# Kernel optimization log

Measured on AMD Instinct MI355X. Metric: run time of the kernel, lower is better.

## Reference

```python
import jax, jax.numpy as jnp
import numpy as np
from jax import lax

B, S, D, T = 128, 512, 512, 64
OUT = 3


def setup_inputs() -> dict:
    key = jax.random.key(0)
    ks = jax.random.split(key, 16)
    sd = 0.05
    return {
        "e_all": jax.random.normal(ks[0], (B, S, D), jnp.float32),
        "e_last": jax.random.normal(ks[1], (1, B, D), jnp.float32),
        "target": jax.random.normal(ks[2], (B, T, OUT), jnp.float32),
        # attention params
        "Wa": jax.random.normal(ks[3], (D, D), jnp.float32) * sd,
        "ba": jnp.zeros((D,), jnp.float32),
        "Ua": jax.random.normal(ks[4], (D, D), jnp.float32) * sd,
        "bu": jnp.zeros((D,), jnp.float32),
        "Va_w": jax.random.normal(ks[5], (1, D), jnp.float32) * sd,
        "Va_b": jnp.zeros((1,), jnp.float32),
        # GRU params (PyTorch layout: [3D, in], gates order r,z,n)
        "W_ih": jax.random.normal(ks[6], (3 * D, D + OUT), jnp.float32) * sd,
        "b_ih": jnp.zeros((3 * D,), jnp.float32),
        "W_hh": jax.random.normal(ks[7], (3 * D, D), jnp.float32) * sd,
        "b_hh": jnp.zeros((3 * D,), jnp.float32),
        # output projection
        "W_out": jax.random.normal(ks[8], (OUT, D), jnp.float32) * sd,
        "b_out": jnp.zeros((OUT,), jnp.float32),
    }


def reference(e_all, e_last, target, Wa, ba, Ua, bu, Va_w, Va_b,
              W_ih, b_ih, W_hh, b_hh, W_out, b_out):
    # Precompute Ua(keys): keys are fixed across timesteps (same math as per-step).
    Uk = jnp.einsum('bsd,ed->bse', e_all, Ua) + bu        # [B,S,D]
    va = Va_w[0]                                          # [D]

    def step(h, x):
        # h: [B,D] decoder hidden; x: [B,3] decoder input (dropout is eval/identity)
        q = h @ Wa.T + ba                                  # [B,D]
        scores = jnp.einsum('bsd,d->bs', jnp.tanh(q[:, None, :] + Uk), va) + Va_b[0]
        w = jax.nn.softmax(scores, axis=-1)                # [B,S]
        ctx = jnp.einsum('bs,bsd->bd', w, e_all)           # [B,D]
        gin = jnp.concatenate([ctx, x], axis=-1)           # [B,D+3]  (attn first)
        gi = gin @ W_ih.T + b_ih                           # [B,3D]
        gh = h @ W_hh.T + b_hh                             # [B,3D]
        i_r, i_z, i_n = jnp.split(gi, 3, axis=-1)
        h_r, h_z, h_n = jnp.split(gh, 3, axis=-1)
        r = jax.nn.sigmoid(i_r + h_r)
        z = jax.nn.sigmoid(i_z + h_z)
        n = jnp.tanh(i_n + r * h_n)
        h_new = (1.0 - z) * n + z * h                      # [B,D]
        out = h_new @ W_out.T + b_out                      # [B,3]
        return h_new, (out, w)

    # teacher forcing: step 0 sees zeros, step i sees target[:, i-1]
    xs = jnp.concatenate([jnp.zeros((1, B, OUT), e_all.dtype),
                          jnp.swapaxes(target[:, :T - 1, :], 0, 1)], axis=0)  # [T,B,3]
    hT, (outs, attns) = lax.scan(step, e_last[0], xs)
    d_outputs = jnp.swapaxes(outs, 0, 1)     # [B,T,3]
    cross_attn = jnp.swapaxes(attns, 0, 1)   # [B,T,S]
    return d_outputs, hT[None], cross_attn
```

## Files before the change

### kernel.cpp

```cpp
#include <hip/hip_runtime.h>
#include <cstdint>

constexpr int BB = 128;
constexpr int SS = 512;
constexpr int DD = 512;
constexpr int TT = 64;
constexpr int OO = 3;

typedef __attribute__((ext_vector_type(8))) short bf16x8;
typedef __attribute__((ext_vector_type(4))) float f32x4;

__device__ __forceinline__ float tanh_fast(float x) {
  float e = __expf(2.0f * x);
  return 1.0f - 2.0f / (e + 1.0f);
}
__device__ __forceinline__ float sigmoid_fast(float x) {
  return 1.0f / (1.0f + __expf(-x));
}
__device__ __forceinline__ unsigned short f2bf(float f) {
  uint32_t u = __float_as_uint(f);
  uint32_t r = (u + 0x7FFFu + ((u >> 16) & 1u)) >> 16;
  return (unsigned short)r;
}
__device__ __forceinline__ float2 bfx2(uint32_t u) {
  float2 r;
  r.x = __uint_as_float(u << 16);
  r.y = __uint_as_float(u & 0xFFFF0000u);
  return r;
}

template<int BM, int BN, int BK, int TM, int TN>
__device__ __forceinline__ void gemm_body(
    const float* __restrict__ A, int lda,
    const float* __restrict__ Bw, int ldb,
    const float* __restrict__ bias,
    float* __restrict__ C, int ldc, int K) {
  constexpr int TX = BN / TN, TY = BM / TM;
  static_assert(TX * TY == 256, "tile/thread mismatch");
  __shared__ float As[BK][BM + 4];
  __shared__ float Bs[BK][BN + 4];
  const int tid = threadIdx.x;
  const int bm = blockIdx.y * BM, bn = blockIdx.x * BN;
  const int tx = tid % TX, ty = tid / TX;
  float acc[TM][TN];
#pragma unroll
  for (int i = 0; i < TM; ++i)
#pragma unroll
    for (int j = 0; j < TN; ++j) acc[i][j] = 0.f;

  for (int k0 = 0; k0 < K; k0 += BK) {
#pragma unroll
    for (int i = 0; i < BM * BK / 256; ++i) {
      int idx = tid + i * 256;
      int m = idx / BK, k = idx % BK;
      As[k][m] = A[(size_t)(bm + m) * lda + k0 + k];
    }
#pragma unroll
    for (int i = 0; i < BN * BK / 256; ++i) {
      int idx = tid + i * 256;
      int n = idx / BK, k = idx % BK;
      Bs[k][n] = Bw[(size_t)(bn + n) * ldb + k0 + k];
    }
    __syncthreads();
#pragma unroll
    for (int k = 0; k < BK; ++k) {
      float ra[TM], rb[TN];
#pragma unroll
      for (int i = 0; i < TM; ++i) ra[i] = As[k][ty * TM + i];
#pragma unroll
      for (int j = 0; j < TN; ++j) rb[j] = Bs[k][tx * TN + j];
#pragma unroll
      for (int i = 0; i < TM; ++i)
#pragma unroll
        for (int j = 0; j < TN; ++j) acc[i][j] += ra[i] * rb[j];
    }
    __syncthreads();
  }
#pragma unroll
  for (int i = 0; i < TM; ++i) {
    int m = bm + ty * TM + i;
#pragma unroll
    for (int j = 0; j < TN; ++j) {
      int n = bn + tx * TN + j;
      C[(size_t)m * ldc + n] = acc[i][j] + bias[n];
    }
  }
}

__global__ __launch_bounds__(256) void gemm_uk_mfma(
    const unsigned short* __restrict__ A, const unsigned short* __restrict__ Bw,
    const float* __restrict__ bias, unsigned short* __restrict__ Uk) {
  __shared__ unsigned short Asb[128 * 40];
  __shared__ unsigned short Bsb[128 * 40];
  const int tid = threadIdx.x;
  const int m0 = blockIdx.y * 128, n0 = blockIdx.x * 128;
  const int w = tid >> 6, l = tid & 63;
  const int wr = w >> 1, wc = w & 1;
  const int lm = l & 15, kg = l >> 4;

  f32x4 acc[4][4] = {};

  for (int kc = 0; kc < 512; kc += 32) {
    uint4 av[2], bv[2];
#pragma unroll
    for (int p = 0; p < 2; ++p) {
      int u = tid + p * 256;
      int r = u >> 2, ko = (u & 3) * 8;
      av[p] = *(const uint4*)(A + (size_t)(m0 + r) * 512 + kc + ko);
      bv[p] = *(const uint4*)(Bw + (size_t)(n0 + r) * 512 + kc + ko);
    }
    __syncthreads();
#pragma unroll
    for (int p = 0; p < 2; ++p) {
      int u = tid + p * 256;
      int r = u >> 2, ko = (u & 3) * 8;
      *(uint4*)&Asb[r * 40 + ko] = av[p];
      *(uint4*)&Bsb[r * 40 + ko] = bv[p];
    }
    __syncthreads();
    bf16x8 af[4], bfr[4];
#pragma unroll
    for (int i = 0; i < 4; ++i) {
      af[i]  = *(const bf16x8*)&Asb[(wr * 64 + i * 16 + lm) * 40 + kg * 8];
      bfr[i] = *(const bf16x8*)&Bsb[(wc * 64 + i * 16 + lm) * 40 + kg * 8];
    }
#pragma unroll
    for (int i = 0; i < 4; ++i)
#pragma unroll
      for (int j = 0; j < 4; ++j)
        acc[i][j] = __builtin_amdgcn_mfma_f32_16x16x32_bf16(af[i], bfr[j],
                                                            acc[i][j], 0, 0, 0);
  }

  const int row_base = m0 + wr * 64;
  const int col_base = n0 + wc * 64;
#pragma unroll
  for (int j = 0; j < 4; ++j) {
    const int col = col_base + j * 16 + lm;
    const float bu = bias[col];
#pragma unroll
    for (int i = 0; i < 4; ++i) {
      const int r0 = row_base + i * 16 + kg * 4;
#pragma unroll
      for (int rr = 0; rr < 4; ++rr)
        Uk[(size_t)(r0 + rr) * 512 + col] = f2bf(acc[i][j][rr] + bu);
    }
  }
}

__global__ __launch_bounds__(256) void conv_bf(const float* __restrict__ in,
                                               unsigned short* __restrict__ outp) {
  size_t idx = ((size_t)blockIdx.x * 256 + threadIdx.x) * 8;
  const float4* p = (const float4*)(in + idx);
  float4 a = p[0], b = p[1];
  uint4 r;
  r.x = f2bf(a.x) | ((uint32_t)f2bf(a.y) << 16);
  r.y = f2bf(a.z) | ((uint32_t)f2bf(a.w) << 16);
  r.z = f2bf(b.x) | ((uint32_t)f2bf(b.y) << 16);
  r.w = f2bf(b.z) | ((uint32_t)f2bf(b.w) << 16);
  *(uint4*)(outp + idx) = r;
}

__global__ void prep_wcat(const float* __restrict__ Wa,
                          const float* __restrict__ Whh,
                          uint32_t* __restrict__ Wcat) {
  int idx = blockIdx.x * 256 + threadIdx.x;
  int k = idx >> 10, j2 = idx & 1023;
  int j0 = 2 * j2;
  float v0 = (j0 < DD) ? Wa[(size_t)j0 * DD + k] : Whh[(size_t)(j0 - DD) * DD + k];
  float v1 = (j0 + 1 < DD) ? Wa[(size_t)(j0 + 1) * DD + k]
                           : Whh[(size_t)(j0 + 1 - DD) * DD + k];
  Wcat[idx] = (uint32_t)f2bf(v0) | ((uint32_t)f2bf(v1) << 16);
}

__global__ void prep_bcat(const float* __restrict__ ba,
                          const float* __restrict__ bhh,
                          float* __restrict__ bcat) {
  int j = blockIdx.x * 256 + threadIdx.x;
  bcat[j] = (j < DD) ? ba[j] : bhh[j - DD];
}

__device__ __forceinline__ void qgh_gemm(
    const float* __restrict__ hn_sh, const uint32_t* __restrict__ Wcat,
    const float* __restrict__ bcat, float* __restrict__ q,
    float* __restrict__ gh, int b, int tid) {
  float2 acc = {0.f, 0.f};
#pragma unroll 8
  for (int k = 0; k < DD; ++k) {
    float2 wv = bfx2(Wcat[(size_t)k * 1024 + tid]);
    float hv = hn_sh[k];
    acc.x += hv * wv.x;
    acc.y += hv * wv.y;
  }
  const int j0 = 2 * tid;
  acc.x += bcat[j0];
  acc.y += bcat[j0 + 1];
  if (j0 < DD) {
    q[(size_t)b * DD + j0] = acc.x;
    q[(size_t)b * DD + j0 + 1] = acc.y;
  } else {
    gh[(size_t)b * 3 * DD + j0 - DD] = acc.x;
    gh[(size_t)b * 3 * DD + j0 + 1 - DD] = acc.y;
  }
}

__global__ __launch_bounds__(1024) void qgh_init(
    const float* __restrict__ e_last, const uint32_t* __restrict__ Wcat,
    const float* __restrict__ bcat, float* __restrict__ h,
    float* __restrict__ q, float* __restrict__ gh) {
  const int b = blockIdx.x, tid = threadIdx.x;
  __shared__ float hn[DD];
  if (tid < DD) {
    float v = e_last[(size_t)b * DD + tid];
    hn[tid] = v;
    h[(size_t)b * DD + tid] = v;
  }
  __syncthreads();
  qgh_gemm(hn, Wcat, bcat, q, gh, b, tid);
}

__global__ __launch_bounds__(256) void attn_scores(
    const unsigned short* __restrict__ Uk_bf, const float* __restrict__ q,
    const float* __restrict__ va, const float* __restrict__ vb_p,
    float* __restrict__ scores) {
  const int b = blockIdx.y;
  const int s0 = blockIdx.x * 64;
  __shared__ float4 shq[DD / 4];
  __shared__ float4 shva[DD / 4];
  const int tid = threadIdx.x;
  if (tid < DD / 4) {
    shq[tid] = ((const float4*)(q + (size_t)b * DD))[tid];
    shva[tid] = ((const float4*)va)[tid];
  }
  __syncthreads();
  const float vb = vb_p[0];
  const int g = tid >> 4, l = tid & 15;
#pragma unroll
  for (int i = 0; i < 4; ++i) {
    const int s = s0 + 16 * i + g;
    const uint4* row = (const uint4*)(Uk_bf + ((size_t)b * SS + s) * DD);
    float acc = 0.f;
#pragma unroll
    for (int jj = 0; jj < 4; ++jj) {
      const int slot = l + 16 * jj;
      uint4 u = row[slot];
      float4 q0 = shq[slot * 2], q1 = shq[slot * 2 + 1];
      float4 v0 = shva[slot * 2], v1 = shva[slot * 2 + 1];
      float2 e0 = bfx2(u.x), e1 = bfx2(u.y), e2 = bfx2(u.z), e3 = bfx2(u.w);
      acc += v0.x * tanh_fast(q0.x + e0.x);
      acc += v0.y * tanh_fast(q0.y + e0.y);
      acc += v0.z * tanh_fast(q0.z + e1.x);
      acc += v0.w * tanh_fast(q0.w + e1.y);
      acc += v1.x * tanh_fast(q1.x + e2.x);
      acc += v1.y * tanh_fast(q1.y + e2.y);
      acc += v1.z * tanh_fast(q1.z + e3.x);
      acc += v1.w * tanh_fast(q1.w + e3.y);
    }
#pragma unroll
    for (int off = 8; off; off >>= 1) acc += __shfl_down(acc, off, 16);
    if (l == 0) scores[(size_t)b * SS + s] = acc + vb;
  }
}

__global__ __launch_bounds__(256) void attn_ctx(
    const unsigned short* __restrict__ e_bf, const float* __restrict__ scores,
    float* __restrict__ ctx, float* __restrict__ attn_out, int t) {
  const int b = blockIdx.y, dc = blockIdx.x;
  __shared__ float w[SS];
  __shared__ float red[8];
  __shared__ float part[16][132];
  const int tid = threadIdx.x;

  float v0 = scores[(size_t)b * SS + tid];
  float v1 = scores[(size_t)b * SS + 256 + tid];
  float m = fmaxf(v0, v1);
#pragma unroll
  for (int off = 32; off; off >>= 1) m = fmaxf(m, __shfl_xor(m, off));
  if ((tid & 63) == 0) red[tid >> 6] = m;
  __syncthreads();
  m = fmaxf(fmaxf(red[0], red[1]), fmaxf(red[2], red[3]));
  float e0 = __expf(v0 - m), e1 = __expf(v1 - m);
  float ss = e0 + e1;
#pragma unroll
  for (int off = 32; off; off >>= 1) ss += __shfl_xor(ss, off);
  __syncthreads();
  if ((tid & 63) == 0) red[tid >> 6] = ss;
  __syncthreads();
  const float inv = 1.f / (red[0] + red[1] + red[2] + red[3]);
  float w0 = e0 * inv, w1 = e1 * inv;
  w[tid] = w0;
  w[tid + 256] = w1;
  if (dc == 0) {
    float* ao = attn_out + ((size_t)b * TT + t) * SS;
    ao[tid] = w0;
    ao[tid + 256] = w1;
  }
  __syncthreads();

  {
    const int sl = tid & 15, sg = tid >> 4;
    const unsigned short* eb = e_bf + (size_t)b * SS * DD + dc * 128 + sl * 8;
    float a0 = 0.f, a1 = 0.f, a2 = 0.f, a3 = 0.f;
    float a4 = 0.f, a5 = 0.f, a6 = 0.f, a7 = 0.f;
    for (int s = sg * 32; s < sg * 32 + 32; ++s) {
      uint4 u = *(const uint4*)(eb + (size_t)s * DD);
      float ws = w[s];
      float2 p0 = bfx2(u.x), p1 = bfx2(u.y), p2 = bfx2(u.z), p3 = bfx2(u.w);
      a0 += ws * p0.x; a1 += ws * p0.y;
      a2 += ws * p1.x; a3 += ws * p1.y;
      a4 += ws * p2.x; a5 += ws * p2.y;
      a6 += ws * p3.x; a7 += ws * p3.y;
    }
    float* pr = &part[sg][sl * 8];
    pr[0] = a0; pr[1] = a1; pr[2] = a2; pr[3] = a3;
    pr[4] = a4; pr[5] = a5; pr[6] = a6; pr[7] = a7;
  }
  __syncthreads();
  if (tid < 128) {
    const int sl = tid >> 3, c = tid & 7;
    float r = 0.f;
#pragma unroll
    for (int sg = 0; sg < 16; ++sg) r += part[sg][sl * 8 + c];
    ctx[(size_t)b * DD + dc * 128 + sl * 8 + c] = r;
  }
}

__global__ __launch_bounds__(256) void gi_gemm(
    const float* __restrict__ ctx, const float* __restrict__ W_ih,
    const float* __restrict__ bih, float* __restrict__ gi) {
  gemm_body<16, 64, 32, 1, 4>(ctx, DD, W_ih, DD + OO, bih, gi, 3 * DD, DD);
}

__global__ __launch_bounds__(1024) void update_fused(
    const float* __restrict__ gi, float* __restrict__ gh,
    float* __restrict__ h,
    const float* __restrict__ W_ih, const float* __restrict__ target,
    const float* __restrict__ W_out, const float* __restrict__ b_out,
    const uint32_t* __restrict__ Wcat, const float* __restrict__ bcat,
    float* __restrict__ q,
    float* __restrict__ out_d, float* __restrict__ out_hT, int t) {
  const int b = blockIdx.x, tid = threadIdx.x;
  __shared__ float hn[DD];
  const int wid = tid >> 6, lane = tid & 63;

  if (tid < DD) {
    const int d = tid;
    float x0 = 0.f, x1 = 0.f, x2 = 0.f;
    if (t > 0) {
      const float* xp = target + ((size_t)b * TT + (t - 1)) * OO;
      x0 = xp[0]; x1 = xp[1]; x2 = xp[2];
    }
    const float* gib = gi + (size_t)b * 3 * DD;
    const float* ghb = gh + (size_t)b * 3 * DD;
    const float* w0 = W_ih + (size_t)d * (DD + OO) + DD;
    const float* w1 = W_ih + (size_t)(DD + d) * (DD + OO) + DD;
    const float* w2 = W_ih + (size_t)(2 * DD + d) * (DD + OO) + DD;
    float ir  = gib[d]          + x0 * w0[0] + x1 * w0[1] + x2 * w0[2];
    float iz  = gib[DD + d]     + x0 * w1[0] + x1 * w1[1] + x2 * w1[2];
    float in_ = gib[2 * DD + d] + x0 * w2[0] + x1 * w2[1] + x2 * w2[2];
    float r = sigmoid_fast(ir + ghb[d]);
    float z = sigmoid_fast(iz + ghb[DD + d]);
    float n = tanh_fast(in_ + r * ghb[2 * DD + d]);
    float hp = h[(size_t)b * DD + d];
    float hnew = (1.f - z) * n + z * hp;
    h[(size_t)b * DD + d] = hnew;
    hn[d] = hnew;
    if (t == TT - 1) out_hT[(size_t)b * DD + d] = hnew;
  }
  __syncthreads();

  if (wid < OO) {
    const float* wrow = W_out + (size_t)wid * DD;
    float acc = 0.f;
    for (int i = lane; i < DD; i += 64) acc += hn[i] * wrow[i];
#pragma unroll
    for (int off = 32; off; off >>= 1) acc += __shfl_xor(acc, off);
    if (lane == 0) out_d[((size_t)b * TT + t) * OO + wid] = acc + b_out[wid];
  }

  qgh_gemm(hn, Wcat, bcat, q, gh, b, tid);
}

extern "C" void kernel_launch(void* const* d_in, const int* in_sizes, int n_in,
                              void* d_out, int out_size, void* d_ws, size_t ws_size,
                              hipStream_t stream) {
  const float* e_all  = (const float*)d_in[0];
  const float* e_last = (const float*)d_in[1];
  const float* target = (const float*)d_in[2];
  const float* Wa     = (const float*)d_in[3];
  const float* ba     = (const float*)d_in[4];
  const float* Ua     = (const float*)d_in[5];
  const float* bu     = (const float*)d_in[6];
  const float* Va_w   = (const float*)d_in[7];
  const float* Va_b   = (const float*)d_in[8];
  const float* W_ih   = (const float*)d_in[9];
  const float* b_ih   = (const float*)d_in[10];
  const float* W_hh   = (const float*)d_in[11];
  const float* b_hh   = (const float*)d_in[12];
  const float* W_out  = (const float*)d_in[13];
  const float* b_out  = (const float*)d_in[14];

  float* out      = (float*)d_out;
  float* out_d    = out;
  float* out_hT   = out + (size_t)BB * TT * OO;
  float* out_attn = out_hT + (size_t)BB * DD;

  char* wsB = (char*)d_ws;
  unsigned short* Uk_bf = (unsigned short*)wsB;
  unsigned short* e_bf  = (unsigned short*)(wsB + (size_t)BB * SS * DD * 2);
  uint32_t* Wcat = (uint32_t*)(wsB + (size_t)BB * SS * DD * 4);
  unsigned short* Ua_bf = (unsigned short*)(wsB + (size_t)BB * SS * DD * 4 +
                                            (size_t)DD * 2048 * 2);
  float* fws = (float*)((char*)Ua_bf + (size_t)DD * DD * 2);
  float* bcat   = fws;
  float* scores = bcat + 2048;
  float* q    = scores + (size_t)BB * SS;
  float* h    = q + (size_t)BB * DD;
  float* ctx  = h + (size_t)BB * DD;
  float* gi   = ctx + (size_t)BB * DD;
  float* gh   = gi + (size_t)BB * 3 * DD;

  prep_wcat<<<(DD * 1024) / 256, 256, 0, stream>>>(Wa, W_hh, Wcat);
  prep_bcat<<<2048 / 256, 256, 0, stream>>>(ba, b_hh, bcat);
  conv_bf<<<(BB * SS * DD) / (8 * 256), 256, 0, stream>>>(e_all, e_bf);
  conv_bf<<<(DD * DD) / (8 * 256), 256, 0, stream>>>(Ua, Ua_bf);
  gemm_uk_mfma<<<dim3(DD / 128, (BB * SS) / 128), 256, 0, stream>>>(
      e_bf, Ua_bf, bu, Uk_bf);
  qgh_init<<<BB, 1024, 0, stream>>>(e_last, Wcat, bcat, h, q, gh);

  for (int t = 0; t < TT; ++t) {
    attn_scores<<<dim3(SS / 64, BB), 256, 0, stream>>>(Uk_bf, q, Va_w, Va_b,
                                                       scores);
    attn_ctx<<<dim3(4, BB), 256, 0, stream>>>(e_bf, scores, ctx, out_attn, t);
    gi_gemm<<<dim3(3 * DD / 64, BB / 16), 256, 0, stream>>>(ctx, W_ih, b_ih, gi);
    update_fused<<<BB, 1024, 0, stream>>>(gi, gh, h, W_ih, target, W_out, b_out,
                                          Wcat, bcat, q, out_d, out_hT, t);
  }
}
```

Baseline: 5.612 ms.

## Fuse the whole decode loop into one persistent per-batch kernel with exp2 tanh

Replaces the 64 × 4 per-step kernel launches with a single persistent kernel that keeps one block per batch row and holds h, q, gh, scores, ctx and gi in shared memory across all timesteps. It also pre-scales Ua/Wa/biases by 2·log2(e), so tanh becomes 1/(1+exp2) folded into the score as -2× a sum, and drops Va_b because softmax is shift-invariant. The gi GEMM now reads a transposed bf16 copy of W_ih instead of the fp32 tiled GEMM. The cost is only 128 blocks on a large GPU, so per-step parallelism is lower than the multi-block launches.

Result: slower. 6.373 ms (+13.6%).

```diff
diff --git a/kernel.cpp b/kernel.cpp
--- a/kernel.cpp
+++ b/kernel.cpp
@@ -7,6 +7,8 @@
 constexpr int TT = 64;
 constexpr int OO = 3;
 
+constexpr float C2LE = 2.8853900817779268f;
+
 typedef __attribute__((ext_vector_type(8))) short bf16x8;
 typedef __attribute__((ext_vector_type(4))) float f32x4;
 
@@ -28,63 +30,19 @@
   r.y = __uint_as_float(u & 0xFFFF0000u);
   return r;
 }
-
-template<int BM, int BN, int BK, int TM, int TN>
-__device__ __forceinline__ void gemm_body(
-    const float* __restrict__ A, int lda,
-    const float* __restrict__ Bw, int ldb,
-    const float* __restrict__ bias,
-    float* __restrict__ C, int ldc, int K) {
-  constexpr int TX = BN / TN, TY = BM / TM;
-  static_assert(TX * TY == 256, "tile/thread mismatch");
-  __shared__ float As[BK][BM + 4];
-  __shared__ float Bs[BK][BN + 4];
-  const int tid = threadIdx.x;
-  const int bm = blockIdx.y * BM, bn = blockIdx.x * BN;
-  const int tx = tid % TX, ty = tid / TX;
-  float acc[TM][TN];
-#pragma unroll
-  for (int i = 0; i < TM; ++i)
-#pragma unroll
-    for (int j = 0; j < TN; ++j) acc[i][j] = 0.f;
-
-  for (int k0 = 0; k0 < K; k0 += BK) {
-#pragma unroll
-    for (int i = 0; i < BM * BK / 256; ++i) {
-      int idx = tid + i * 256;
-      int m = idx / BK, k = idx % BK;
-      As[k][m] = A[(size_t)(bm + m) * lda + k0 + k];
-    }
-#pragma unroll
-    for (int i = 0; i < BN * BK / 256; ++i) {
-      int idx = tid + i * 256;
-      int n = idx / BK, k = idx % BK;
-      Bs[k][n] = Bw[(size_t)(bn + n) * ldb + k0 + k];
-    }
-    __syncthreads();
-#pragma unroll
-    for (int k = 0; k < BK; ++k) {
-      float ra[TM], rb[TN];
-#pragma unroll
-      for (int i = 0; i < TM; ++i) ra[i] = As[k][ty * TM + i];
-#pragma unroll
-      for (int j = 0; j < TN; ++j) rb[j] = Bs[k][tx * TN + j];
-#pragma unroll
-      for (int i = 0; i < TM; ++i)
-#pragma unroll
-        for (int j = 0; j < TN; ++j) acc[i][j] += ra[i] * rb[j];
-    }
-    __syncthreads();
-  }
-#pragma unroll
-  for (int i = 0; i < TM; ++i) {
-    int m = bm + ty * TM + i;
-#pragma unroll
-    for (int j = 0; j < TN; ++j) {
-      int n = bn + tx * TN + j;
-      C[(size_t)m * ldc + n] = acc[i][j] + bias[n];
-    }
-  }
+__device__ __forceinline__ float fexp2(float x) {
+#if __has_builtin(__builtin_amdgcn_exp2f)
+  return __builtin_amdgcn_exp2f(x);
+#else
+  return exp2f(x);
+#endif
+}
+__device__ __forceinline__ float frcp(float x) {
+#if __has_builtin(__builtin_amdgcn_rcpf)
+  return __builtin_amdgcn_rcpf(x);
+#else
+  return 1.0f / x;
+#endif
 }
 
 __global__ __launch_bounds__(256) void gemm_uk_mfma(
@@ -143,7 +101,7 @@
       const int r0 = row_base + i * 16 + kg * 4;
 #pragma unroll
       for (int rr = 0; rr < 4; ++rr)
-        Uk[(size_t)(r0 + rr) * 512 + col] = f2bf(acc[i][j][rr] + bu);
+        Uk[(size_t)(r0 + rr) * 512 + col] = f2bf(C2LE * (acc[i][j][rr] + bu));
     }
   }
 }
@@ -167,8 +125,9 @@
   int idx = blockIdx.x * 256 + threadIdx.x;
   int k = idx >> 10, j2 = idx & 1023;
   int j0 = 2 * j2;
-  float v0 = (j0 < DD) ? Wa[(size_t)j0 * DD + k] : Whh[(size_t)(j0 - DD) * DD + k];
-  float v1 = (j0 + 1 < DD) ? Wa[(size_t)(j0 + 1) * DD + k]
+  float v0 = (j0 < DD) ? Wa[(size_t)j0 * DD + k] * C2LE
+                       : Whh[(size_t)(j0 - DD) * DD + k];
+  float v1 = (j0 + 1 < DD) ? Wa[(size_t)(j0 + 1) * DD + k] * C2LE
                            : Whh[(size_t)(j0 + 1 - DD) * DD + k];
   Wcat[idx] = (uint32_t)f2bf(v0) | ((uint32_t)f2bf(v1) << 16);
 }
@@ -177,208 +136,224 @@
                           const float* __restrict__ bhh,
                           float* __restrict__ bcat) {
   int j = blockIdx.x * 256 + threadIdx.x;
-  bcat[j] = (j < DD) ? ba[j] : bhh[j - DD];
-}
-
-__device__ __forceinline__ void qgh_gemm(
-    const float* __restrict__ hn_sh, const uint32_t* __restrict__ Wcat,
-    const float* __restrict__ bcat, float* __restrict__ q,
-    float* __restrict__ gh, int b, int tid) {
-  float2 acc = {0.f, 0.f};
-#pragma unroll 8
-  for (int k = 0; k < DD; ++k) {
-    float2 wv = bfx2(Wcat[(size_t)k * 1024 + tid]);
-    float hv = hn_sh[k];
-    acc.x += hv * wv.x;
-    acc.y += hv * wv.y;
+  bcat[j] = (j < DD) ? ba[j] * C2LE : bhh[j - DD];
+}
+
+__global__ void prep_wih(const float* __restrict__ W_ih,
+                         uint32_t* __restrict__ Wih2) {
+  int idx = blockIdx.x * 256 + threadIdx.x;
+  int k = idx / 768, j2 = idx % 768;
+  int j0 = 2 * j2;
+  float v0 = W_ih[(size_t)j0 * (DD + OO) + k];
+  float v1 = W_ih[(size_t)(j0 + 1) * (DD + OO) + k];
+  Wih2[(size_t)k * 768 + j2] = (uint32_t)f2bf(v0) | ((uint32_t)f2bf(v1) << 16);
+}
+
+__device__ __forceinline__ void qgh_phase(const float* h_sh,
+                                          const uint32_t* __restrict__ Wcat,
+                                          const float* __restrict__ bcat,
+                                          float* q2_sh, float* gh_sh, int tid) {
+  float ax = 0.f, ay = 0.f;
+  for (int k0 = 0; k0 < DD; k0 += 8) {
+    float hk[8];
+    *(float4*)&hk[0] = *(const float4*)&h_sh[k0];
+    *(float4*)&hk[4] = *(const float4*)&h_sh[k0 + 4];
+#pragma unroll
+    for (int kk = 0; kk < 8; ++kk) {
+      float2 w2 = bfx2(Wcat[(size_t)(k0 + kk) * 1024 + tid]);
+      ax += hk[kk] * w2.x;
+      ay += hk[kk] * w2.y;
+    }
   }
   const int j0 = 2 * tid;
-  acc.x += bcat[j0];
-  acc.y += bcat[j0 + 1];
+  ax += bcat[j0];
+  ay += bcat[j0 + 1];
   if (j0 < DD) {
-    q[(size_t)b * DD + j0] = acc.x;
-    q[(size_t)b * DD + j0 + 1] = acc.y;
+    q2_sh[j0] = ax;
+    q2_sh[j0 + 1] = ay;
   } else {
-    gh[(size_t)b * 3 * DD + j0 - DD] = acc.x;
-    gh[(size_t)b * 3 * DD + j0 + 1 - DD] = acc.y;
-  }
-}
-
-__global__ __launch_bounds__(1024) void qgh_init(
-    const float* __restrict__ e_last, const uint32_t* __restrict__ Wcat,
-    const float* __restrict__ bcat, float* __restrict__ h,
-    float* __restrict__ q, float* __restrict__ gh) {
+    gh_sh[j0 - DD] = ax;
+    gh_sh[j0 + 1 - DD] = ay;
+  }
+}
+
+__global__ __launch_bounds__(1024, 1) void decode_persistent(
+    const unsigned short* __restrict__ Uk2, const unsigned short* __restrict__ e_bf,
+    const uint32_t* __restrict__ Wcat, const float* __restrict__ bcat,
+    const uint32_t* __restrict__ Wih2, const float* __restrict__ b_ih,
+    const float* __restrict__ W_ih, const float* __restrict__ e_last,
+    const float* __restrict__ target, const float* __restrict__ Va_w,
+    const float* __restrict__ W_out, const float* __restrict__ b_out,
+    float* __restrict__ out_d, float* __restrict__ out_hT,
+    float* __restrict__ out_attn) {
   const int b = blockIdx.x, tid = threadIdx.x;
-  __shared__ float hn[DD];
+
+  __shared__ float h_s[DD];
+  __shared__ float q2_s[DD];
+  __shared__ float va_s[DD];
+  __shared__ float sc_s[SS];
+  __shared__ float w_s[SS];
+  __shared__ float ctx_s[DD];
+  __shared__ float gi_s[3 * DD];
+  __shared__ float gh_s[3 * DD];
+  __shared__ float red_s[32];
+  __shared__ float part_s[16 * 520];
+
   if (tid < DD) {
-    float v = e_last[(size_t)b * DD + tid];
-    hn[tid] = v;
-    h[(size_t)b * DD + tid] = v;
+    h_s[tid] = e_last[(size_t)b * DD + tid];
+    va_s[tid] = Va_w[tid];
   }
   __syncthreads();
-  qgh_gemm(hn, Wcat, bcat, q, gh, b, tid);
-}
-
-__global__ __launch_bounds__(256) void attn_scores(
-    const unsigned short* __restrict__ Uk_bf, const float* __restrict__ q,
-    const float* __restrict__ va, const float* __restrict__ vb_p,
-    float* __restrict__ scores) {
-  const int b = blockIdx.y;
-  const int s0 = blockIdx.x * 64;
-  __shared__ float4 shq[DD / 4];
-  __shared__ float4 shva[DD / 4];
-  const int tid = threadIdx.x;
-  if (tid < DD / 4) {
-    shq[tid] = ((const float4*)(q + (size_t)b * DD))[tid];
-    shva[tid] = ((const float4*)va)[tid];
-  }
+  qgh_phase(h_s, Wcat, bcat, q2_s, gh_s, tid);
   __syncthreads();
-  const float vb = vb_p[0];
-  const int g = tid >> 4, l = tid & 15;
-#pragma unroll
-  for (int i = 0; i < 4; ++i) {
-    const int s = s0 + 16 * i + g;
-    const uint4* row = (const uint4*)(Uk_bf + ((size_t)b * SS + s) * DD);
-    float acc = 0.f;
-#pragma unroll
-    for (int jj = 0; jj < 4; ++jj) {
-      const int slot = l + 16 * jj;
-      uint4 u = row[slot];
-      float4 q0 = shq[slot * 2], q1 = shq[slot * 2 + 1];
-      float4 v0 = shva[slot * 2], v1 = shva[slot * 2 + 1];
-      float2 e0 = bfx2(u.x), e1 = bfx2(u.y), e2 = bfx2(u.z), e3 = bfx2(u.w);
-      acc += v0.x * tanh_fast(q0.x + e0.x);
-      acc += v0.y * tanh_fast(q0.y + e0.y);
-      acc += v0.z * tanh_fast(q0.z + e1.x);
-      acc += v0.w * tanh_fast(q0.w + e1.y);
-      acc += v1.x * tanh_fast(q1.x + e2.x);
-      acc += v1.y * tanh_fast(q1.y + e2.y);
-      acc += v1.z * tanh_fast(q1.z + e3.x);
-      acc += v1.w * tanh_fast(q1.w + e3.y);
-    }
-#pragma unroll
-    for (int off = 8; off; off >>= 1) acc += __shfl_down(acc, off, 16);
-    if (l == 0) scores[(size_t)b * SS + s] = acc + vb;
-  }
-}
-
-__global__ __launch_bounds__(256) void attn_ctx(
-    const unsigned short* __restrict__ e_bf, const float* __restrict__ scores,
-    float* __restrict__ ctx, float* __restrict__ attn_out, int t) {
-  const int b = blockIdx.y, dc = blockIdx.x;
-  __shared__ float w[SS];
-  __shared__ float red[8];
-  __shared__ float part[16][132];
-  const int tid = threadIdx.x;
-
-  float v0 = scores[(size_t)b * SS + tid];
-  float v1 = scores[(size_t)b * SS + 256 + tid];
-  float m = fmaxf(v0, v1);
-#pragma unroll
-  for (int off = 32; off; off >>= 1) m = fmaxf(m, __shfl_xor(m, off));
-  if ((tid & 63) == 0) red[tid >> 6] = m;
-  __syncthreads();
-  m = fmaxf(fmaxf(red[0], red[1]), fmaxf(red[2], red[3]));
-  float e0 = __expf(v0 - m), e1 = __expf(v1 - m);
-  float ss = e0 + e1;
-#pragma unroll
-  for (int off = 32; off; off >>= 1) ss += __shfl_xor(ss, off);
-  __syncthreads();
-  if ((tid & 63) == 0) red[tid >> 6] = ss;
-  __syncthreads();
-  const float inv = 1.f / (red[0] + red[1] + red[2] + red[3]);
-  float w0 = e0 * inv, w1 = e1 * inv;
-  w[tid] = w0;
-  w[tid + 256] = w1;
-  if (dc == 0) {
-    float* ao = attn_out + ((size_t)b * TT + t) * SS;
-    ao[tid] = w0;
-    ao[tid + 256] = w1;
-  }
-  __syncthreads();
-
-  {
-    const int sl = tid & 15, sg = tid >> 4;
-    const unsigned short* eb = e_bf + (size_t)b * SS * DD + dc * 128 + sl * 8;
-    float a0 = 0.f, a1 = 0.f, a2 = 0.f, a3 = 0.f;
-    float a4 = 0.f, a5 = 0.f, a6 = 0.f, a7 = 0.f;
-    for (int s = sg * 32; s < sg * 32 + 32; ++s) {
-      uint4 u = *(const uint4*)(eb + (size_t)s * DD);
-      float ws = w[s];
-      float2 p0 = bfx2(u.x), p1 = bfx2(u.y), p2 = bfx2(u.z), p3 = bfx2(u.w);
-      a0 += ws * p0.x; a1 += ws * p0.y;
-      a2 += ws * p1.x; a3 += ws * p1.y;
-      a4 += ws * p2.x; a5 += ws * p2.y;
-      a6 += ws * p3.x; a7 += ws * p3.y;
-    }
-    float* pr = &part[sg][sl * 8];
-    pr[0] = a0; pr[1] = a1; pr[2] = a2; pr[3] = a3;
-    pr[4] = a4; pr[5] = a5; pr[6] = a6; pr[7] = a7;
-  }
-  __syncthreads();
-  if (tid < 128) {
-    const int sl = tid >> 3, c = tid & 7;
-    float r = 0.f;
-#pragma unroll
-    for (int sg = 0; sg < 16; ++sg) r += part[sg][sl * 8 + c];
-    ctx[(size_t)b * DD + dc * 128 + sl * 8 + c] = r;
-  }
-}
-
-__global__ __launch_bounds__(256) void gi_gemm(
-    const float* __restrict__ ctx, const float* __restrict__ W_ih,
-    const float* __restrict__ bih, float* __restrict__ gi) {
-  gemm_body<16, 64, 32, 1, 4>(ctx, DD, W_ih, DD + OO, bih, gi, 3 * DD, DD);
-}
-
-__global__ __launch_bounds__(1024) void update_fused(
-    const float* __restrict__ gi, float* __restrict__ gh,
-    float* __restrict__ h,
-    const float* __restrict__ W_ih, const float* __restrict__ target,
-    const float* __restrict__ W_out, const float* __restrict__ b_out,
-    const uint32_t* __restrict__ Wcat, const float* __restrict__ bcat,
-    float* __restrict__ q,
-    float* __restrict__ out_d, float* __restrict__ out_hT, int t) {
-  const int b = blockIdx.x, tid = threadIdx.x;
-  __shared__ float hn[DD];
-  const int wid = tid >> 6, lane = tid & 63;
-
-  if (tid < DD) {
-    const int d = tid;
-    float x0 = 0.f, x1 = 0.f, x2 = 0.f;
-    if (t > 0) {
-      const float* xp = target + ((size_t)b * TT + (t - 1)) * OO;
-      x0 = xp[0]; x1 = xp[1]; x2 = xp[2];
-    }
-    const float* gib = gi + (size_t)b * 3 * DD;
-    const float* ghb = gh + (size_t)b * 3 * DD;
-    const float* w0 = W_ih + (size_t)d * (DD + OO) + DD;
-    const float* w1 = W_ih + (size_t)(DD + d) * (DD + OO) + DD;
-    const float* w2 = W_ih + (size_t)(2 * DD + d) * (DD + OO) + DD;
-    float ir  = gib[d]          + x0 * w0[0] + x1 * w0[1] + x2 * w0[2];
-    float iz  = gib[DD + d]     + x0 * w1[0] + x1 * w1[1] + x2 * w1[2];
-    float in_ = gib[2 * DD + d] + x0 * w2[0] + x1 * w2[1] + x2 * w2[2];
-    float r = sigmoid_fast(ir + ghb[d]);
-    float z = sigmoid_fast(iz + ghb[DD + d]);
-    float n = tanh_fast(in_ + r * ghb[2 * DD + d]);
-    float hp = h[(size_t)b * DD + d];
-    float hnew = (1.f - z) * n + z * hp;
-    h[(size_t)b * DD + d] = hnew;
-    hn[d] = hnew;
-    if (t == TT - 1) out_hT[(size_t)b * DD + d] = hnew;
-  }
-  __syncthreads();
-
-  if (wid < OO) {
-    const float* wrow = W_out + (size_t)wid * DD;
-    float acc = 0.f;
-    for (int i = lane; i < DD; i += 64) acc += hn[i] * wrow[i];
-#pragma unroll
-    for (int off = 32; off; off >>= 1) acc += __shfl_xor(acc, off);
-    if (lane == 0) out_d[((size_t)b * TT + t) * OO + wid] = acc + b_out[wid];
-  }
-
-  qgh_gemm(hn, Wcat, bcat, q, gh, b, tid);
+
+  for (int t = 0; t < TT; ++t) {
+    {
+      const int s = tid >> 1, hf = tid & 1;
+      const uint4* up =
+          (const uint4*)(Uk2 + ((size_t)b * SS + s) * DD + hf * 256);
+      const float4* qp = (const float4*)&q2_s[hf * 256];
+      const float4* vp = (const float4*)&va_s[hf * 256];
+      float acc = 0.f;
+#pragma unroll 4
+      for (int j = 0; j < 32; ++j) {
+        uint4 u = up[j];
+        float4 q0 = qp[2 * j], q1 = qp[2 * j + 1];
+        float4 v0 = vp[2 * j], v1 = vp[2 * j + 1];
+        float2 e0 = bfx2(u.x), e1 = bfx2(u.y), e2 = bfx2(u.z), e3 = bfx2(u.w);
+        acc += v0.x * frcp(1.f + fexp2(q0.x + e0.x));
+        acc += v0.y * frcp(1.f + fexp2(q0.y + e0.y));
+        acc += v0.z * frcp(1.f + fexp2(q0.z + e1.x));
+        acc += v0.w * frcp(1.f + fexp2(q0.w + e1.y));
+        acc += v1.x * frcp(1.f + fexp2(q1.x + e2.x));
+        acc += v1.y * frcp(1.f + fexp2(q1.y + e2.y));
+        acc += v1.z * frcp(1.f + fexp2(q1.z + e3.x));
+        acc += v1.w * frcp(1.f + fexp2(q1.w + e3.y));
+      }
+      acc += __shfl_xor(acc, 1);
+      if (hf == 0) sc_s[s] = acc;
+    }
+    __syncthreads();
+
+    float yv = 0.f, ev = 0.f;
+    {
+      float m = -1e30f;
+      if (tid < SS) {
+        yv = -2.f * sc_s[tid];
+        m = yv;
+      }
+#pragma unroll
+      for (int off = 32; off; off >>= 1) m = fmaxf(m, __shfl_xor(m, off));
+      if ((tid & 63) == 0) red_s[tid >> 6] = m;
+    }
+    __syncthreads();
+    {
+      float gm = red_s[0];
+#pragma unroll
+      for (int i = 1; i < 8; ++i) gm = fmaxf(gm, red_s[i]);
+      float sm = 0.f;
+      if (tid < SS) {
+        ev = __expf(yv - gm);
+        sm = ev;
+      }
+#pragma unroll
+      for (int off = 32; off; off >>= 1) sm += __shfl_xor(sm, off);
+      if ((tid & 63) == 0) red_s[16 + (tid >> 6)] = sm;
+    }
+    __syncthreads();
+    {
+      float tot = red_s[16];
+#pragma unroll
+      for (int i = 1; i < 8; ++i) tot += red_s[16 + i];
+      if (tid < SS) {
+        float wv = ev * frcp(tot);
+        w_s[tid] = wv;
+        out_attn[((size_t)b * TT + t) * SS + tid] = wv;
+      }
+    }
+    __syncthreads();
+
+    {
+      const int wv = tid >> 6, ln = tid & 63;
+      const unsigned short* eb = e_bf + (size_t)b * SS * DD + ln * 8;
+      float a0 = 0.f, a1 = 0.f, a2 = 0.f, a3 = 0.f;
+      float a4 = 0.f, a5 = 0.f, a6 = 0.f, a7 = 0.f;
+#pragma unroll 4
+      for (int si = 0; si < 32; ++si) {
+        const int s = wv * 32 + si;
+        uint4 u = *(const uint4*)(eb + (size_t)s * DD);
+        float ws = w_s[s];
+        float2 p0 = bfx2(u.x), p1 = bfx2(u.y), p2 = bfx2(u.z), p3 = bfx2(u.w);
+        a0 += ws * p0.x; a1 += ws * p0.y;
+        a2 += ws * p1.x; a3 += ws * p1.y;
+        a4 += ws * p2.x; a5 += ws * p2.y;
+        a6 += ws * p3.x; a7 += ws * p3.y;
+      }
+      float4 lo = {a0, a1, a2, a3}, hi = {a4, a5, a6, a7};
+      *(float4*)&part_s[wv * 520 + ln * 8] = lo;
+      *(float4*)&part_s[wv * 520 + ln * 8 + 4] = hi;
+    }
+    __syncthreads();
+    if (tid < DD) {
+      float r = 0.f;
+#pragma unroll
+      for (int sg = 0; sg < 16; ++sg) r += part_s[sg * 520 + tid];
+      ctx_s[tid] = r;
+    }
+    __syncthreads();
+
+    if (tid < 768) {
+      float ax = 0.f, ay = 0.f;
+      for (int k0 = 0; k0 < DD; k0 += 8) {
+        float ck[8];
+        *(float4*)&ck[0] = *(const float4*)&ctx_s[k0];
+        *(float4*)&ck[4] = *(const float4*)&ctx_s[k0 + 4];
+#pragma unroll
+        for (int kk = 0; kk < 8; ++kk) {
+          float2 w2 = bfx2(Wih2[(size_t)(k0 + kk) * 768 + tid]);
+          ax += ck[kk] * w2.x;
+          ay += ck[kk] * w2.y;
+        }
+      }
+      gi_s[2 * tid] = ax + b_ih[2 * tid];
+      gi_s[2 * tid + 1] = ay + b_ih[2 * tid + 1];
+    }
+    __syncthreads();
+
+    if (tid < DD) {
+      const int d = tid;
+      float x0 = 0.f, x1 = 0.f, x2 = 0.f;
+      if (t > 0) {
+        const float* xp = target + ((size_t)b * TT + (t - 1)) * OO;
+        x0 = xp[0]; x1 = xp[1]; x2 = xp[2];
+      }
+      const float* w0 = W_ih + (size_t)d * (DD + OO) + DD;
+      const float* w1 = W_ih + (size_t)(DD + d) * (DD + OO) + DD;
+      const float* w2 = W_ih + (size_t)(2 * DD + d) * (DD + OO) + DD;
+      float ir  = gi_s[d]          + x0 * w0[0] + x1 * w0[1] + x2 * w0[2];
+      float iz  = gi_s[DD + d]     + x0 * w1[0] + x1 * w1[1] + x2 * w1[2];
+      float in_ = gi_s[2 * DD + d] + x0 * w2[0] + x1 * w2[1] + x2 * w2[2];
+      float r = sigmoid_fast(ir + gh_s[d]);
+      float z = sigmoid_fast(iz + gh_s[DD + d]);
+      float n = tanh_fast(in_ + r * gh_s[2 * DD + d]);
+      float hnew = (1.f - z) * n + z * h_s[d];
+      h_s[d] = hnew;
+      if (t == TT - 1) out_hT[(size_t)b * DD + d] = hnew;
+    }
+    __syncthreads();
+
+    if (tid < 192) {
+      const int wid = tid >> 6, ln = tid & 63;
+      const float* wrow = W_out + (size_t)wid * DD;
+      float acc = 0.f;
+      for (int i = ln; i < DD; i += 64) acc += h_s[i] * wrow[i];
+#pragma unroll
+      for (int off = 32; off; off >>= 1) acc += __shfl_xor(acc, off);
+      if (ln == 0) out_d[((size_t)b * TT + t) * OO + wid] = acc + b_out[wid];
+    }
+    qgh_phase(h_s, Wcat, bcat, q2_s, gh_s, tid);
+    __syncthreads();
+  }
 }
 
 extern "C" void kernel_launch(void* const* d_in, const int* in_sizes, int n_in,
@@ -392,7 +367,6 @@
   const float* Ua     = (const float*)d_in[5];
   const float* bu     = (const float*)d_in[6];
   const float* Va_w   = (const float*)d_in[7];
-  const float* Va_b   = (const float*)d_in[8];
   const float* W_ih   = (const float*)d_in[9];
   const float* b_ih   = (const float*)d_in[10];
   const float* W_hh   = (const float*)d_in[11];
@@ -406,34 +380,25 @@
   float* out_attn = out_hT + (size_t)BB * DD;
 
   char* wsB = (char*)d_ws;
-  unsigned short* Uk_bf = (unsigned short*)wsB;
-  unsigned short* e_bf  = (unsigned short*)(wsB + (size_t)BB * SS * DD * 2);
-  uint32_t* Wcat = (uint32_t*)(wsB + (size_t)BB * SS * DD * 4);
-  unsigned short* Ua_bf = (unsigned short*)(wsB + (size_t)BB * SS * DD * 4 +
-                                            (size_t)DD * 2048 * 2);
-  float* fws = (float*)((char*)Ua_bf + (size_t)DD * DD * 2);
-  float* bcat   = fws;
-  float* scores = bcat + 2048;
-  float* q    = scores + (size_t)BB * SS;
-  float* h    = q + (size_t)BB * DD;
-  float* ctx  = h + (size_t)BB * DD;
-  float* gi   = ctx + (size_t)BB * DD;
-  float* gh   = gi + (size_t)BB * 3 * DD;
+  const size_t szUk = (size_t)BB * SS * DD * 2;
+  unsigned short* Uk2   = (unsigned short*)wsB;
+  unsigned short* e_bfp = (unsigned short*)(wsB + szUk);
+  uint32_t* Wcat = (uint32_t*)(wsB + 2 * szUk);
+  uint32_t* Wih2 = (uint32_t*)(wsB + 2 * szUk + (size_t)DD * 1024 * 4);
+  unsigned short* Ua_bf = (unsigned short*)(wsB + 2 * szUk +
+                                            (size_t)DD * 1024 * 4 +
+                                            (size_t)DD * 768 * 4);
+  float* bcat = (float*)((char*)Ua_bf + (size_t)DD * DD * 2);
 
   prep_wcat<<<(DD * 1024) / 256, 256, 0, stream>>>(Wa, W_hh, Wcat);
   prep_bcat<<<2048 / 256, 256, 0, stream>>>(ba, b_hh, bcat);
-  conv_bf<<<(BB * SS * DD) / (8 * 256), 256, 0, stream>>>(e_all, e_bf);
+  prep_wih<<<(DD * 768) / 256, 256, 0, stream>>>(W_ih, Wih2);
+  conv_bf<<<(BB * SS * DD) / (8 * 256), 256, 0, stream>>>(e_all, e_bfp);
   conv_bf<<<(DD * DD) / (8 * 256), 256, 0, stream>>>(Ua, Ua_bf);
   gemm_uk_mfma<<<dim3(DD / 128, (BB * SS) / 128), 256, 0, stream>>>(
-      e_bf, Ua_bf, bu, Uk_bf);
-  qgh_init<<<BB, 1024, 0, stream>>>(e_last, Wcat, bcat, h, q, gh);
-
-  for (int t = 0; t < TT; ++t) {
-    attn_scores<<<dim3(SS / 64, BB), 256, 0, stream>>>(Uk_bf, q, Va_w, Va_b,
-                                                       scores);
-    attn_ctx<<<dim3(4, BB), 256, 0, stream>>>(e_bf, scores, ctx, out_attn, t);
-    gi_gemm<<<dim3(3 * DD / 64, BB / 16), 256, 0, stream>>>(ctx, W_ih, b_ih, gi);
-    update_fused<<<BB, 1024, 0, stream>>>(gi, gh, h, W_ih, target, W_out, b_out,
-                                          Wcat, bcat, q, out_d, out_hT, t);
-  }
-}
+      e_bfp, Ua_bf, bu, Uk2);
+
+  decode_persistent<<<BB, 1024, 0, stream>>>(
+      Uk2, e_bfp, Wcat, bcat, Wih2, b_ih, W_ih, e_last, target, Va_w,
+      W_out, b_out, out_d, out_hT, out_attn);
+}
```
